# Performance work log

Hardware: AMD Instinct MI355X
Metric: run time of the kernel (lower is better)

## Reference

```python
import jax, jax.numpy as jnp
import numpy as np

E, T, K, N = 8, 8192, 2048, 4096  # experts, total tokens, hidden, ffn-out


def setup_inputs() -> dict:
    key = jax.random.key(0)
    k1, k2, k3, k4 = jax.random.split(key, 4)
    a = jax.random.normal(k1, (T, K), dtype=jnp.float32)
    # weight_column_major=True layout: [num_experts, N, K]
    b = jax.random.normal(k2, (E, N, K), dtype=jnp.float32) * 0.02
    c = jnp.zeros((T, N), dtype=jnp.float32)  # preallocated output buffer
    # monotone segment offsets: 0 = p0 <= p1 <= ... <= pE = T
    cuts = jnp.sort(jax.random.randint(k3, (E - 1,), 0, T))
    seg_indptr = jnp.concatenate([
        jnp.zeros((1,), jnp.int64),
        cuts.astype(jnp.int64),
        jnp.full((1,), T, jnp.int64),
    ])
    weight_indices = jax.random.permutation(k4, E).astype(jnp.int64)
    return {
        "a": a,
        "b": b,
        "c": c,
        "batch_size": E,
        "weight_column_major": 1,
        "seg_indptr": seg_indptr,
        "weight_indices": weight_indices,
    }


def reference(a, b, c, batch_size, weight_column_major, seg_indptr, weight_indices):
    # Grouped GEMM: for each segment s, c[p_s:p_{s+1}] = a[p_s:p_{s+1}] @ b[widx[s]].T
    group_sizes = jnp.diff(seg_indptr).astype(jnp.int32)  # [E]
    # gather per-segment weights and convert column-major [E,N,K] -> [E,K,N]
    rhs = jnp.swapaxes(b[weight_indices], 1, 2)
    return jax.lax.ragged_dot(a, rhs, group_sizes)  # [T, N]
```

## Files before the change

### kernel.cpp

```cpp
#include <hip/hip_runtime.h>
#include <stdint.h>
#include <stddef.h>


typedef __attribute__((ext_vector_type(8))) short short8;
typedef __attribute__((ext_vector_type(4))) float floatx4;

constexpr int E_c = 8;
constexpr int T_c = 8192;
constexpr int K_c = 2048;
constexpr int N_c = 4096;
constexpr int BM = 128;
constexpr int BN = 128;
constexpr int BK = 32;
constexpr int KSTEPS = K_c / BK;
constexpr int XTILES = T_c / BM + E_c;
constexpr int YTILES = N_c / BN;

__device__ __forceinline__ uint32_t pack2(float lo, float hi) {
  union { float f; uint32_t u; } a, b;
  a.f = lo; b.f = hi;
  return __builtin_amdgcn_perm(b.u, a.u, 0x07060302u);
}

__global__ __launch_bounds__(256) void cvt_both_kernel(
    const float* __restrict__ A, const float* __restrict__ Bm,
    ushort* __restrict__ dst) {
  const int n8A = T_c * K_c / 8;
  const int n8T = n8A + E_c * N_c * K_c / 8;
  int i = blockIdx.x * 256 + threadIdx.x;
  const int stride = gridDim.x * 256;
  for (; i < n8T; i += stride) {
    const float* s =
        (i < n8A) ? A + (size_t)i * 8 : Bm + (size_t)(i - n8A) * 8;
    float4 v0 = ((const float4*)s)[0], v1 = ((const float4*)s)[1];
    int4 o;
    o.x = pack2(v0.x, v0.y); o.y = pack2(v0.z, v0.w);
    o.z = pack2(v1.x, v1.y); o.w = pack2(v1.z, v1.w);
    ((int4*)dst)[i] = o;
  }
}

__device__ __forceinline__ void gload16(const ushort* g, ushort* l) {
  __builtin_amdgcn_global_load_lds(
      (const __attribute__((address_space(1))) unsigned int*)g,
      (__attribute__((address_space(3))) unsigned int*)l, 16, 0, 0);
}

__global__ __launch_bounds__(256) void grouped_gemm_bf16_kernel(
    const ushort* __restrict__ A, const ushort* __restrict__ B,
    const int* __restrict__ segp, const int* __restrict__ widx,
    float* __restrict__ C) {
  __shared__ ushort As0[BM * BK], As1[BM * BK], As2[BM * BK];
  __shared__ ushort Bs0[BN * BK], Bs1[BN * BK], Bs2[BN * BK];

  const int t = threadIdx.x;

  const int bid = blockIdx.x;
  const int xcd = bid & 7;
  const int i = bid >> 3;
  const int yl = i / XTILES;
  const int x = i - yl * XTILES;
  const int y = xcd * 4 + yl;

  int s = -1, r0i = 0, rendi = 0, acc_t = 0;
#pragma unroll
  for (int e = 0; e < E_c; ++e) {
    int pe = segp[e], pe1 = segp[e + 1];
    int nt = (pe1 - pe + BM - 1) >> 7;
    if (s < 0 && (x - acc_t) < nt) {
      s = e;
      r0i = pe + ((x - acc_t) << 7);
      rendi = pe1;
    }
    acc_t += nt;
  }
  if (s < 0) return;
  const int expert = widx[s];
  const int n0 = y * BN;

  const int wave = t >> 6;
  const int gc = (((t & 3) ^ ((t >> 3) & 3)) << 3);
  int ar0 = r0i + (t >> 2);
  int ar1 = ar0 + 64;
  if (ar0 > T_c - 1) ar0 = T_c - 1;
  if (ar1 > T_c - 1) ar1 = T_c - 1;
  const ushort* Ag0 = A + (size_t)ar0 * K_c + gc;
  const ushort* Ag1 = A + (size_t)ar1 * K_c + gc;
  const ushort* Bg0 = B + ((size_t)expert * N_c + n0 + (t >> 2)) * K_c + gc;
  const ushort* Bg1 = Bg0 + (size_t)64 * K_c;
  const int lo0 = wave * 512;
  const int lo1 = 2048 + wave * 512;

  const int lane = t & 63;
  const int m16 = lane & 15;
  const int quad = lane >> 4;
  const int csw = (quad ^ ((m16 >> 1) & 3)) << 3;
  const int wm = (wave & 1) << 6;
  const int wn = (wave >> 1) << 6;
  int ia[4], ib[4];
#pragma unroll
  for (int q = 0; q < 4; ++q) {
    ia[q] = (wm + q * 16 + m16) * BK + csw;
    ib[q] = (wn + q * 16 + m16) * BK + csw;
  }

  floatx4 acc[4][4];
#pragma unroll
  for (int p = 0; p < 4; ++p)
#pragma unroll
    for (int q = 0; q < 4; ++q) acc[p][q] = (floatx4){0.f, 0.f, 0.f, 0.f};

#define STAGE(Asb, Bsb, kc)                                              \
  {                                                                      \
    const int ko = (kc)*BK;                                              \
    gload16(Ag0 + ko, (Asb) + lo0);                                      \
    gload16(Ag1 + ko, (Asb) + lo1);                                      \
    gload16(Bg0 + ko, (Bsb) + lo0);                                      \
    gload16(Bg1 + ko, (Bsb) + lo1);                                      \
  }

#define COMPUTE(Asb, Bsb)                                                \
  {                                                                      \
    short8 aF[4], bF[4];                                                 \
    _Pragma("unroll") for (int q = 0; q < 4; ++q) {                      \
      aF[q] = *(const short8*)&(Asb)[ia[q]];                             \
      bF[q] = *(const short8*)&(Bsb)[ib[q]];                             \
    }                                                                    \
    __builtin_amdgcn_s_setprio(1);                                       \
    _Pragma("unroll") for (int p = 0; p < 4; ++p)                        \
        _Pragma("unroll") for (int q = 0; q < 4; ++q) acc[p][q] =        \
        __builtin_amdgcn_mfma_f32_16x16x32_bf16(aF[p], bF[q], acc[p][q], \
                                                0, 0, 0);                \
    __builtin_amdgcn_s_setprio(0);                                       \
  }

#define STEPBAR()                                                        \
  asm volatile("s_waitcnt vmcnt(4) lgkmcnt(0)" ::: "memory");            \
  __builtin_amdgcn_s_barrier();

  STAGE(As0, Bs0, 0);
  STAGE(As1, Bs1, 1);
  asm volatile("s_waitcnt vmcnt(4)" ::: "memory");
  __builtin_amdgcn_s_barrier();

#pragma unroll 1
  for (int k = 0; k < KSTEPS - 1; k += 3) {
    STAGE(As2, Bs2, k + 2);
    COMPUTE(As0, Bs0);
    STEPBAR();
    STAGE(As0, Bs0, (k + 3 < KSTEPS) ? k + 3 : KSTEPS - 1);
    COMPUTE(As1, Bs1);
    STEPBAR();
    STAGE(As1, Bs1, (k + 4 < KSTEPS) ? k + 4 : KSTEPS - 1);
    COMPUTE(As2, Bs2);
    STEPBAR();
  }
  COMPUTE(As0, Bs0);

#undef STAGE
#undef COMPUTE
#undef STEPBAR

#pragma unroll
  for (int p = 0; p < 4; ++p) {
    int growb = r0i + wm + p * 16 + quad * 4;
#pragma unroll
    for (int q = 0; q < 4; ++q) {
      int gcol = n0 + wn + q * 16 + m16;
#pragma unroll
      for (int rr = 0; rr < 4; ++rr) {
        int grow = growb + rr;
        if (grow < rendi) C[(size_t)grow * N_c + gcol] = acc[p][q][rr];
      }
    }
  }
}

constexpr int LSTR = 5;

__device__ __forceinline__ void cvt16(const float4* p, int4* c0, int4* c1) {
  c0->x = pack2(p[0].x, p[0].y); c0->y = pack2(p[0].z, p[0].w);
  c0->z = pack2(p[1].x, p[1].y); c0->w = pack2(p[1].z, p[1].w);
  c1->x = pack2(p[2].x, p[2].y); c1->y = pack2(p[2].z, p[2].w);
  c1->z = pack2(p[3].x, p[3].y); c1->w = pack2(p[3].z, p[3].w);
}

__global__ __launch_bounds__(256) void grouped_gemm_fallback(
    const float* __restrict__ A, const float* __restrict__ B,
    const int* __restrict__ segp, const int* __restrict__ widx,
    float* __restrict__ C) {
  __shared__ int4 As[BM * LSTR];
  __shared__ int4 Bs[BN * LSTR];

  const int t = threadIdx.x;
  const int bid = blockIdx.x;
  const int xcd = bid & 7;
  const int i = bid >> 3;
  const int yl = i / XTILES;
  const int x = i - yl * XTILES;
  const int y = xcd * 4 + yl;

  int s = -1, r0i = 0, rendi = 0, acc_t = 0;
#pragma unroll
  for (int e = 0; e < E_c; ++e) {
    int pe = segp[e], pe1 = segp[e + 1];
    int nt = (pe1 - pe + BM - 1) >> 7;
    if (s < 0 && (x - acc_t) < nt) {
      s = e;
      r0i = pe + ((x - acc_t) << 7);
      rendi = pe1;
    }
    acc_t += nt;
  }
  if (s < 0) return;
  const int expert = widx[s];
  const int n0 = y * BN;

  const int r = t >> 1;
  const int h = t & 1;
  int arow = r0i + r;
  if (arow > T_c - 1) arow = T_c - 1;
  const float* Abase = A + (size_t)arow * K_c + h * 16;
  const float* Bbase = B + ((size_t)expert * N_c + n0 + r) * K_c + h * 16;
  const int wI = r * LSTR + 2 * h;

  const int lane = t & 63;
  const int wave = t >> 6;
  const int m16 = lane & 15;
  const int quad = lane >> 4;
  const int wm = (wave & 1) << 6;
  const int wn = (wave >> 1) << 6;
  int ia[4], ib[4];
#pragma unroll
  for (int q = 0; q < 4; ++q) {
    ia[q] = (wm + q * 16 + m16) * LSTR + quad;
    ib[q] = (wn + q * 16 + m16) * LSTR + quad;
  }

  floatx4 acc[4][4];
#pragma unroll
  for (int p = 0; p < 4; ++p)
#pragma unroll
    for (int q = 0; q < 4; ++q) acc[p][q] = (floatx4){0.f, 0.f, 0.f, 0.f};

  float4 pa[4], pb[4];
#pragma unroll
  for (int j = 0; j < 4; ++j) {
    pa[j] = ((const float4*)Abase)[j];
    pb[j] = ((const float4*)Bbase)[j];
  }

#pragma unroll 1
  for (int kt = 0; kt < 64; ++kt) {
    __syncthreads();
    int4 a0, a1, b0, b1;
    cvt16(pa, &a0, &a1);
    cvt16(pb, &b0, &b1);
    As[wI] = a0; As[wI + 1] = a1;
    Bs[wI] = b0; Bs[wI + 1] = b1;
    __syncthreads();

    const int knext = (kt + 1 < 64) ? kt + 1 : 63;
    const float* an = Abase + knext * 32;
    const float* bn = Bbase + knext * 32;
#pragma unroll
    for (int j = 0; j < 4; ++j) {
      pa[j] = ((const float4*)an)[j];
      pb[j] = ((const float4*)bn)[j];
    }

    short8 aF[4], bF[4];
#pragma unroll
    for (int q = 0; q < 4; ++q) {
      aF[q] = *(const short8*)&As[ia[q]];
      bF[q] = *(const short8*)&Bs[ib[q]];
    }
#pragma unroll
    for (int p = 0; p < 4; ++p)
#pragma unroll
      for (int q = 0; q < 4; ++q)
        acc[p][q] = __builtin_amdgcn_mfma_f32_16x16x32_bf16(aF[p], bF[q],
                                                            acc[p][q], 0, 0, 0);
  }

#pragma unroll
  for (int p = 0; p < 4; ++p) {
    int growb = r0i + wm + p * 16 + quad * 4;
#pragma unroll
    for (int q = 0; q < 4; ++q) {
      int gcol = n0 + wn + q * 16 + m16;
#pragma unroll
      for (int rr = 0; rr < 4; ++rr) {
        int grow = growb + rr;
        if (grow < rendi) C[(size_t)grow * N_c + gcol] = acc[p][q][rr];
      }
    }
  }
}

extern "C" void kernel_launch(void* const* d_in, const int* in_sizes, int n_in,
                              void* d_out, int out_size, void* d_ws, size_t ws_size,
                              hipStream_t stream) {
  const float* A = (const float*)d_in[0];
  const float* B = (const float*)d_in[1];
  const int* segp = (const int*)d_in[5];
  const int* widx = (const int*)d_in[6];
  float* C = (float*)d_out;

  const size_t abytes = (size_t)T_c * K_c * 2;
  const size_t bbytes = (size_t)E_c * N_c * K_c * 2;

  if (ws_size >= abytes + bbytes) {
    ushort* Abf = (ushort*)d_ws;
    ushort* Bbf = Abf + (size_t)T_c * K_c;
    cvt_both_kernel<<<2048, 256, 0, stream>>>(A, B, Abf);
    grouped_gemm_bf16_kernel<<<dim3(XTILES * YTILES), 256, 0, stream>>>(
        Abf, Bbf, segp, widx, C);
  } else {
    grouped_gemm_fallback<<<dim3(XTILES * YTILES), 256, 0, stream>>>(
        A, B, segp, widx, C);
  }
}
```

Baseline: 725.1 us.

## Enlarge GEMM tiles to 256x256 with 512 threads and 4-stage pipeline

```diff
diff --git a/kernel.cpp b/kernel.cpp
--- a/kernel.cpp
+++ b/kernel.cpp
@@ -10,12 +10,14 @@
 constexpr int T_c = 8192;
 constexpr int K_c = 2048;
 constexpr int N_c = 4096;
-constexpr int BM = 128;
-constexpr int BN = 128;
+
+constexpr int BM = 256;
+constexpr int BN = 256;
 constexpr int BK = 32;
-constexpr int KSTEPS = K_c / BK;
+constexpr int NK = K_c / BK;
 constexpr int XTILES = T_c / BM + E_c;
 constexpr int YTILES = N_c / BN;
+constexpr int TSZ = BM * BK;
 
 __device__ __forceinline__ uint32_t pack2(float lo, float hi) {
   union { float f; uint32_t u; } a, b;
@@ -47,30 +49,30 @@
       (__attribute__((address_space(3))) unsigned int*)l, 16, 0, 0);
 }
 
-__global__ __launch_bounds__(256) void grouped_gemm_bf16_kernel(
+__global__ __launch_bounds__(512, 2) void grouped_gemm_bf16_kernel(
     const ushort* __restrict__ A, const ushort* __restrict__ B,
     const int* __restrict__ segp, const int* __restrict__ widx,
     float* __restrict__ C) {
-  __shared__ ushort As0[BM * BK], As1[BM * BK], As2[BM * BK];
-  __shared__ ushort Bs0[BN * BK], Bs1[BN * BK], Bs2[BN * BK];
+  __shared__ ushort As0[TSZ], As1[TSZ], As2[TSZ], As3[TSZ];
+  __shared__ ushort Bs0[TSZ], Bs1[TSZ], Bs2[TSZ], Bs3[TSZ];
 
   const int t = threadIdx.x;
 
   const int bid = blockIdx.x;
   const int xcd = bid & 7;
-  const int i = bid >> 3;
-  const int yl = i / XTILES;
-  const int x = i - yl * XTILES;
-  const int y = xcd * 4 + yl;
+  const int bi = bid >> 3;
+  const int yl = bi / XTILES;
+  const int x = bi - yl * XTILES;
+  const int y = xcd * 2 + yl;
 
   int s = -1, r0i = 0, rendi = 0, acc_t = 0;
 #pragma unroll
   for (int e = 0; e < E_c; ++e) {
     int pe = segp[e], pe1 = segp[e + 1];
-    int nt = (pe1 - pe + BM - 1) >> 7;
+    int nt = (pe1 - pe + BM - 1) >> 8;
     if (s < 0 && (x - acc_t) < nt) {
       s = e;
-      r0i = pe + ((x - acc_t) << 7);
+      r0i = pe + ((x - acc_t) << 8);
       rendi = pe1;
     }
     acc_t += nt;
@@ -79,95 +81,110 @@
   const int expert = widx[s];
   const int n0 = y * BN;
 
-  const int wave = t >> 6;
-  const int gc = (((t & 3) ^ ((t >> 3) & 3)) << 3);
-  int ar0 = r0i + (t >> 2);
-  int ar1 = ar0 + 64;
-  if (ar0 > T_c - 1) ar0 = T_c - 1;
-  if (ar1 > T_c - 1) ar1 = T_c - 1;
-  const ushort* Ag0 = A + (size_t)ar0 * K_c + gc;
-  const ushort* Ag1 = A + (size_t)ar1 * K_c + gc;
-  const ushort* Bg0 = B + ((size_t)expert * N_c + n0 + (t >> 2)) * K_c + gc;
-  const ushort* Bg1 = Bg0 + (size_t)64 * K_c;
-  const int lo0 = wave * 512;
-  const int lo1 = 2048 + wave * 512;
-
+  const int w = t >> 6;
   const int lane = t & 63;
+  const int rl = lane >> 2;
+  const int gc = (((lane & 3) ^ ((lane >> 3) & 3)) << 3);
+  int arA0 = r0i + w * 16 + rl;
+  int arA1 = arA0 + 128;
+  if (arA0 > T_c - 1) arA0 = T_c - 1;
+  if (arA1 > T_c - 1) arA1 = T_c - 1;
+  const ushort* AgJ0 = A + (size_t)arA0 * K_c + gc;
+  const ushort* AgJ1 = A + (size_t)arA1 * K_c + gc;
+  const ushort* BgJ0 =
+      B + ((size_t)expert * N_c + n0 + w * 16 + rl) * K_c + gc;
+  const ushort* BgJ1 = BgJ0 + (size_t)128 * K_c;
+  const int lw0 = w * 512;
+  const int lw1 = 4096 + w * 512;
+
   const int m16 = lane & 15;
   const int quad = lane >> 4;
   const int csw = (quad ^ ((m16 >> 1) & 3)) << 3;
-  const int wm = (wave & 1) << 6;
-  const int wn = (wave >> 1) << 6;
-  int ia[4], ib[4];
+  const int wr = w >> 2;
+  const int wc = w & 3;
+  int iaL[4], iaH[4], ib[4];
 #pragma unroll
   for (int q = 0; q < 4; ++q) {
-    ia[q] = (wm + q * 16 + m16) * BK + csw;
-    ib[q] = (wn + q * 16 + m16) * BK + csw;
-  }
-
-  floatx4 acc[4][4];
-#pragma unroll
-  for (int p = 0; p < 4; ++p)
+    iaL[q] = (wr * 128 + q * 16 + m16) * BK + csw;
+    iaH[q] = (wr * 128 + 64 + q * 16 + m16) * BK + csw;
+    ib[q] = (wc * 64 + q * 16 + m16) * BK + csw;
+  }
+
+  floatx4 acc[8][4];
+#pragma unroll
+  for (int p = 0; p < 8; ++p)
 #pragma unroll
     for (int q = 0; q < 4; ++q) acc[p][q] = (floatx4){0.f, 0.f, 0.f, 0.f};
 
-#define STAGE(Asb, Bsb, kc)                                              \
+#define STAGEPAIR(Asb, Bsb, kt)                                          \
   {                                                                      \
-    const int ko = (kc)*BK;                                              \
-    gload16(Ag0 + ko, (Asb) + lo0);                                      \
-    gload16(Ag1 + ko, (Asb) + lo1);                                      \
-    gload16(Bg0 + ko, (Bsb) + lo0);                                      \
-    gload16(Bg1 + ko, (Bsb) + lo1);                                      \
-  }
-
-#define COMPUTE(Asb, Bsb)                                                \
+    const size_t ko = (size_t)(kt)*BK;                                   \
+    gload16(AgJ0 + ko, (Asb) + lw0);                                     \
+    gload16(AgJ1 + ko, (Asb) + lw1);                                     \
+    gload16(BgJ0 + ko, (Bsb) + lw0);                                     \
+    gload16(BgJ1 + ko, (Bsb) + lw1);                                     \
+  }
+
+#define STEP(Asb, Bsb, Asn, Bsn, ktn)                                    \
   {                                                                      \
+    const size_t ko = (size_t)(ktn)*BK;                                  \
     short8 aF[4], bF[4];                                                 \
     _Pragma("unroll") for (int q = 0; q < 4; ++q) {                      \
-      aF[q] = *(const short8*)&(Asb)[ia[q]];                             \
+      aF[q] = *(const short8*)&(Asb)[iaL[q]];                            \
       bF[q] = *(const short8*)&(Bsb)[ib[q]];                             \
     }                                                                    \
+    gload16(AgJ0 + ko, (Asn) + lw0);                                     \
+    gload16(AgJ1 + ko, (Asn) + lw1);                                     \
     __builtin_amdgcn_s_setprio(1);                                       \
     _Pragma("unroll") for (int p = 0; p < 4; ++p)                        \
         _Pragma("unroll") for (int q = 0; q < 4; ++q) acc[p][q] =        \
         __builtin_amdgcn_mfma_f32_16x16x32_bf16(aF[p], bF[q], acc[p][q], \
                                                 0, 0, 0);                \
     __builtin_amdgcn_s_setprio(0);                                       \
-  }
-
-#define STEPBAR()                                                        \
-  asm volatile("s_waitcnt vmcnt(4) lgkmcnt(0)" ::: "memory");            \
+    __builtin_amdgcn_s_barrier();                                        \
+    short8 aG[4];                                                        \
+    _Pragma("unroll") for (int q = 0; q < 4; ++q) aG[q] =                \
+        *(const short8*)&(Asb)[iaH[q]];                                  \
+    gload16(BgJ0 + ko, (Bsn) + lw0);                                     \
+    gload16(BgJ1 + ko, (Bsn) + lw1);                                     \
+    __builtin_amdgcn_s_setprio(1);                                       \
+    _Pragma("unroll") for (int p = 0; p < 4; ++p)                        \
+        _Pragma("unroll") for (int q = 0; q < 4; ++q) acc[p + 4][q] =    \
+        __builtin_amdgcn_mfma_f32_16x16x32_bf16(aG[p], bF[q],            \
+                                                acc[p + 4][q], 0, 0, 0); \
+    __builtin_amdgcn_s_setprio(0);                                       \
+    asm volatile("s_waitcnt vmcnt(8)" ::: "memory");                     \
+    __builtin_amdgcn_s_barrier();                                        \
+  }
+
+  STAGEPAIR(As0, Bs0, 0);
+  STAGEPAIR(As1, Bs1, 1);
+  STAGEPAIR(As2, Bs2, 2);
+  asm volatile("s_waitcnt vmcnt(8)" ::: "memory");
   __builtin_amdgcn_s_barrier();
 
-  STAGE(As0, Bs0, 0);
-  STAGE(As1, Bs1, 1);
-  asm volatile("s_waitcnt vmcnt(4)" ::: "memory");
-  __builtin_amdgcn_s_barrier();
-
 #pragma unroll 1
-  for (int k = 0; k < KSTEPS - 1; k += 3) {
-    STAGE(As2, Bs2, k + 2);
-    COMPUTE(As0, Bs0);
-    STEPBAR();
-    STAGE(As0, Bs0, (k + 3 < KSTEPS) ? k + 3 : KSTEPS - 1);
-    COMPUTE(As1, Bs1);
-    STEPBAR();
-    STAGE(As1, Bs1, (k + 4 < KSTEPS) ? k + 4 : KSTEPS - 1);
-    COMPUTE(As2, Bs2);
-    STEPBAR();
-  }
-  COMPUTE(As0, Bs0);
-
-#undef STAGE
-#undef COMPUTE
-#undef STEPBAR
-
-#pragma unroll
-  for (int p = 0; p < 4; ++p) {
-    int growb = r0i + wm + p * 16 + quad * 4;
+  for (int kb = 0; kb < NK / 4; ++kb) {
+    const int k4 = kb * 4;
+    const int n3 = (k4 + 3 < NK) ? k4 + 3 : NK - 1;
+    const int n4 = (k4 + 4 < NK) ? k4 + 4 : NK - 1;
+    const int n5 = (k4 + 5 < NK) ? k4 + 5 : NK - 1;
+    const int n6 = (k4 + 6 < NK) ? k4 + 6 : NK - 1;
+    STEP(As0, Bs0, As3, Bs3, n3);
+    STEP(As1, Bs1, As0, Bs0, n4);
+    STEP(As2, Bs2, As1, Bs1, n5);
+    STEP(As3, Bs3, As2, Bs2, n6);
+  }
+
+#undef STAGEPAIR
+#undef STEP
+
+#pragma unroll
+  for (int p = 0; p < 8; ++p) {
+    int growb = r0i + wr * 128 + p * 16 + quad * 4;
 #pragma unroll
     for (int q = 0; q < 4; ++q) {
-      int gcol = n0 + wn + q * 16 + m16;
+      int gcol = n0 + wc * 64 + q * 16 + m16;
 #pragma unroll
       for (int rr = 0; rr < 4; ++rr) {
         int grow = growb + rr;
@@ -177,6 +194,9 @@
   }
 }
 
+constexpr int FBM = 128;
+constexpr int FXT = T_c / FBM + E_c;
+constexpr int FYT = N_c / FBM;
 constexpr int LSTR = 5;
 
 __device__ __forceinline__ void cvt16(const float4* p, int4* c0, int4* c1) {
@@ -190,22 +210,22 @@
     const float* __restrict__ A, const float* __restrict__ B,
     const int* __restrict__ segp, const int* __restrict__ widx,
     float* __restrict__ C) {
-  __shared__ int4 As[BM * LSTR];
-  __shared__ int4 Bs[BN * LSTR];
+  __shared__ int4 As[FBM * LSTR];
+  __shared__ int4 Bs[FBM * LSTR];
 
   const int t = threadIdx.x;
   const int bid = blockIdx.x;
   const int xcd = bid & 7;
   const int i = bid >> 3;
-  const int yl = i / XTILES;
-  const int x = i - yl * XTILES;
+  const int yl = i / FXT;
+  const int x = i - yl * FXT;
   const int y = xcd * 4 + yl;
 
   int s = -1, r0i = 0, rendi = 0, acc_t = 0;
 #pragma unroll
   for (int e = 0; e < E_c; ++e) {
     int pe = segp[e], pe1 = segp[e + 1];
-    int nt = (pe1 - pe + BM - 1) >> 7;
+    int nt = (pe1 - pe + FBM - 1) >> 7;
     if (s < 0 && (x - acc_t) < nt) {
       s = e;
       r0i = pe + ((x - acc_t) << 7);
@@ -215,7 +235,7 @@
   }
   if (s < 0) return;
   const int expert = widx[s];
-  const int n0 = y * BN;
+  const int n0 = y * FBM;
 
   const int r = t >> 1;
   const int h = t & 1;
@@ -231,11 +251,11 @@
   const int quad = lane >> 4;
   const int wm = (wave & 1) << 6;
   const int wn = (wave >> 1) << 6;
-  int ia[4], ib[4];
+  int ia[4], ib2[4];
 #pragma unroll
   for (int q = 0; q < 4; ++q) {
     ia[q] = (wm + q * 16 + m16) * LSTR + quad;
-    ib[q] = (wn + q * 16 + m16) * LSTR + quad;
+    ib2[q] = (wn + q * 16 + m16) * LSTR + quad;
   }
 
   floatx4 acc[4][4];
@@ -274,7 +294,7 @@
 #pragma unroll
     for (int q = 0; q < 4; ++q) {
       aF[q] = *(const short8*)&As[ia[q]];
-      bF[q] = *(const short8*)&Bs[ib[q]];
+      bF[q] = *(const short8*)&Bs[ib2[q]];
     }
 #pragma unroll
     for (int p = 0; p < 4; ++p)
@@ -315,10 +335,10 @@
     ushort* Abf = (ushort*)d_ws;
     ushort* Bbf = Abf + (size_t)T_c * K_c;
     cvt_both_kernel<<<2048, 256, 0, stream>>>(A, B, Abf);
-    grouped_gemm_bf16_kernel<<<dim3(XTILES * YTILES), 256, 0, stream>>>(
+    grouped_gemm_bf16_kernel<<<dim3(XTILES * YTILES), 512, 0, stream>>>(
         Abf, Bbf, segp, widx, C);
   } else {
-    grouped_gemm_fallback<<<dim3(XTILES * YTILES), 256, 0, stream>>>(
+    grouped_gemm_fallback<<<dim3(FXT * FYT), 256, 0, stream>>>(
         A, B, segp, widx, C);
   }
 }
```

After: 699.0 us. 3.6% less time.
